# Optimization experiments

Hardware: AMD Instinct MI355X
Metric: run time of the kernel (lower is better)

## Reference

```python
import jax, jax.numpy as jnp
import numpy as np

EPS = 1e-8
BETA = 0.02          # bisector-band sharpness
ALPHA_UNION = 8.0    # exp-union strength
W_MIN, W_MAX = 0.005, 0.5
RAW_TEMP = 5.0       # width squash temperature
REL_TEMP = 0.05      # seed-relevance softmax temperature
A_MIN, A_MAX = 0.5, 2.0  # anisotropy eigenvalue range


def setup_inputs() -> dict:
    key = jax.random.key(0)
    k1, k2, k3, k4, k5 = jax.random.split(key, 5)
    N, S = 65536, 32
    return {
        "points_uv": jax.random.uniform(k1, (N, 2), dtype=jnp.float32),
        "seeds_raw": jax.random.uniform(k2, (S, 2), dtype=jnp.float32),
        "w_raw": jax.random.normal(k3, (1,), dtype=jnp.float32),
        "theta": jax.random.normal(k4, (S,), dtype=jnp.float32),
        "a_raw": jax.random.normal(k5, (S,), dtype=jnp.float32),
    }


def _metric_matrices(theta, a_raw):
    # anisotropic 2x2 SPD metrics M_s = R^T diag(a, 1/a) R
    t = jnp.tanh(a_raw)
    a = 0.5 * (A_MAX - A_MIN) * t + 0.5 * (A_MAX + A_MIN)  # (S,)
    c, s = jnp.cos(theta), jnp.sin(theta)
    R = jnp.stack([jnp.stack([c, -s], -1), jnp.stack([s, c], -1)], -2)  # (S,2,2)
    dvec = jnp.stack([a, 1.0 / (a + EPS)], -1)  # (S,2)
    return jnp.einsum("ska,sk,skb->sab", R, dvec, R)  # (S,2,2)


def reference(points_uv, seeds_raw, w_raw, theta, a_raw):
    S = seeds_raw.shape[0]
    # half-thickness around the Voronoi bisector
    w = W_MIN + (W_MAX - W_MIN) * jax.nn.sigmoid(w_raw[0] / RAW_TEMP)
    M = _metric_matrices(theta, a_raw)  # (S,2,2)

    # point-to-seed diffs with periodic wrapping on both u and v
    diff = points_uv[:, None, :] - seeds_raw[None, :, :]  # (N,S,2)
    diff = diff - jnp.round(diff)

    # anisotropic distances d_i(x) = sqrt(diff^T M_i diff)
    d = jnp.sqrt(jnp.einsum("nsa,sab,nsb->ns", diff, M, diff) + EPS)  # (N,S)

    # soft seed relevance -> soft pair weights P_ij (upper triangular, normalized)
    w_soft = jax.nn.softmax(-d / REL_TEMP, axis=1)  # (N,S)
    pair = w_soft[:, :, None] * w_soft[:, None, :]  # (N,S,S)
    mask = jnp.triu(jnp.ones((S, S), dtype=points_uv.dtype), k=1)
    pair = pair * mask
    P = pair / (pair.sum(axis=(1, 2), keepdims=True) + EPS)

    # bisector band: B_ij = sigmoid((w - |d_i - d_j|_smooth) / beta)
    Delta = d[:, :, None] - d[:, None, :]  # (N,S,S)
    abs_smooth = jnp.sqrt(Delta * Delta + EPS)
    B = jax.nn.sigmoid((w - abs_smooth) / BETA)

    # union over i<j pairs: rho = 1 - exp(-alpha * sum S_ij)
    S_sum = jnp.sum(P * B, axis=(1, 2))  # (N,)
    rho = 1.0 - jnp.exp(-ALPHA_UNION * S_sum)
    return rho
```

## Files before the change

kernel.cpp:

```cpp
#include <hip/hip_runtime.h>
#include <math.h>


#define LOG2E  1.4426950408889634f
#define EPSF   1e-8f
#define TSC    4096.0f
#define TAB_N  2816
#define HBAND  750
#define BLOCK  512
#define PPB    64
#define SSTR   40

__global__ __launch_bounds__(BLOCK, 8) void voronoi_v7(
    const float* __restrict__ points,
    const float* __restrict__ seeds,
    const float* __restrict__ w_raw,
    const float* __restrict__ theta,
    const float* __restrict__ a_raw,
    float* __restrict__ out,
    int N)
{
    __shared__ float    s_tab[TAB_N];
    __shared__ unsigned s_ii[PPB * SSTR];
    __shared__ float    s_ww[PPB * SSTR];
    __shared__ float    s_su[32], s_sv[32], s_m00[32], s_m01[32], s_m11[32];

    const int t = threadIdx.x;

    const float wr = w_raw[0];
    const float sg = __builtin_amdgcn_rcpf(1.0f + exp2f(wr * (-LOG2E / 5.0f)));
    const float w  = 0.005f + 0.495f * sg;

    const int icent = (int)(w * TSC + 0.5f);
    const int T1B   = (icent > HBAND ? icent - HBAND : 0) << 2;
    const int T2B   = (icent + HBAND) << 2;

    if (t < 32) {
        const float x  = a_raw[t];
        const float z  = exp2f(2.0f * LOG2E * x);
        const float th = (z - 1.0f) * __builtin_amdgcn_rcpf(z + 1.0f);
        const float a  = 0.75f * th + 1.25f;
        const float ia = __builtin_amdgcn_rcpf(a + EPSF);
        const float cs = __cosf(theta[t]);
        const float sn = __sinf(theta[t]);
        const float S2 = TSC * TSC;
        s_m00[t] = (a * cs * cs + ia * sn * sn) * S2;
        s_m01[t] = (2.0f * cs * sn * (ia - a)) * S2;
        s_m11[t] = (a * sn * sn + ia * cs * cs) * S2;
        s_su[t]  = seeds[2 * t];
        s_sv[t]  = seeds[2 * t + 1];
    }
    {
        const float kC = (50.0f * LOG2E) / TSC;
        const float kB = -w * (50.0f * LOG2E);
        #pragma unroll
        for (int k = t; k < TAB_N; k += BLOCK) {
            const float y = exp2f(fmaf((float)k, kC, kB));
            s_tab[k] = __builtin_amdgcn_rcpf(1.0f + y);
        }
    }
    __syncthreads();

    const int pb = t >> 3;
    const int g  = t & 7;
    const int s0 = g * 4;
    const int p  = blockIdx.x * PPB + pb;
    if (p >= N) return;

    const float4 su4  = *(const float4*)&s_su[s0];
    const float4 sv4  = *(const float4*)&s_sv[s0];
    const float4 m004 = *(const float4*)&s_m00[s0];
    const float4 m014 = *(const float4*)&s_m01[s0];
    const float4 m114 = *(const float4*)&s_m11[s0];

    const float2 uv = ((const float2*)points)[p];
    const float u = uv.x, v = uv.y;

    const float EPS_Q = 1e-8f * TSC * TSC;
    float4 d4;
#define DIST(SU, SV, M00, M01, M11, OUTD)                                  \
    {                                                                      \
        float du = u - (SU); du -= rintf(du);                              \
        float dv = v - (SV); dv -= rintf(dv);                              \
        float q = fmaf(du * du, (M00),                                     \
                  fmaf(du * dv, (M01),                                     \
                  fmaf(dv * dv, (M11), EPS_Q)));                           \
        (OUTD) = sqrtf(q);                                                 \
    }
    DIST(su4.x, sv4.x, m004.x, m014.x, m114.x, d4.x)
    DIST(su4.y, sv4.y, m004.y, m014.y, m114.y, d4.y)
    DIST(su4.z, sv4.z, m004.z, m014.z, m114.z, d4.z)
    DIST(su4.w, sv4.w, m004.w, m014.w, m114.w, d4.w)

    const float cE = -(20.0f * LOG2E) / TSC;
    float4 e4;
    e4.x = exp2f(d4.x * cE);
    e4.y = exp2f(d4.y * cE);
    e4.z = exp2f(d4.z * cE);
    e4.w = exp2f(d4.w * cE);
    float Z = (e4.x + e4.y) + (e4.z + e4.w);
    Z += __shfl_xor(Z, 1, 64);
    Z += __shfl_xor(Z, 2, 64);
    Z += __shfl_xor(Z, 4, 64);
    const float rcpZ = __builtin_amdgcn_rcpf(Z);
    float4 w4;
    w4.x = e4.x * rcpZ; w4.y = e4.y * rcpZ;
    w4.z = e4.z * rcpZ; w4.w = e4.w * rcpZ;
    float sumsq = w4.x * w4.x;
    sumsq = fmaf(w4.y, w4.y, sumsq);
    sumsq = fmaf(w4.z, w4.z, sumsq);
    sumsq = fmaf(w4.w, w4.w, sumsq);

    uint4 ii;
    ii.x = ((unsigned)(d4.x + 0.5f)) << 2;
    ii.y = ((unsigned)(d4.y + 0.5f)) << 2;
    ii.z = ((unsigned)(d4.z + 0.5f)) << 2;
    ii.w = ((unsigned)(d4.w + 0.5f)) << 2;

    unsigned* db = &s_ii[pb * SSTR];
    float*    wb = &s_ww[pb * SSTR];
    *(uint4*) (db + s0) = ii;
    *(float4*)(wb + s0) = w4;

    const char* tb = (const char*)s_tab;

#define TBODY(IA, IB, WJ, ACC)                                             \
    {                                                                      \
        const unsigned hi = (IA) > (IB) ? (IA) : (IB);                     \
        const unsigned lo = (IA) > (IB) ? (IB) : (IA);                     \
        int diff = (int)(hi - lo);                                         \
        diff = diff > T1B ? diff : T1B;                                    \
        diff = diff < T2B ? diff : T2B;                                    \
        const float B = *(const float*)(tb + diff);                        \
        (ACC) = fmaf((WJ), B, (ACC));                                      \
    }

    float b0, b1, b2, b3;
    b0 = 0.0f; b1 = 0.0f; b2 = 0.0f; b3 = 0.0f;
    TBODY(ii.x, ii.y, w4.y, b0)
    TBODY(ii.x, ii.z, w4.z, b0)
    TBODY(ii.x, ii.w, w4.w, b0)
    TBODY(ii.y, ii.z, w4.z, b1)
    TBODY(ii.y, ii.w, w4.w, b1)
    TBODY(ii.z, ii.w, w4.w, b2)

#define ROT(R)                                                             \
    {                                                                      \
        const int gj = ((g + (R)) & 7) * 4;                                \
        const uint4  ij = *(const uint4*) (db + gj);                       \
        const float4 wj = *(const float4*)(wb + gj);                       \
        TBODY(ii.x, ij.x, wj.x, b0)                                        \
        TBODY(ii.x, ij.y, wj.y, b0)                                        \
        TBODY(ii.x, ij.z, wj.z, b0)                                        \
        TBODY(ii.x, ij.w, wj.w, b0)                                        \
        TBODY(ii.y, ij.x, wj.x, b1)                                        \
        TBODY(ii.y, ij.y, wj.y, b1)                                        \
        TBODY(ii.y, ij.z, wj.z, b1)                                        \
        TBODY(ii.y, ij.w, wj.w, b1)                                        \
        TBODY(ii.z, ij.x, wj.x, b2)                                        \
        TBODY(ii.z, ij.y, wj.y, b2)                                        \
        TBODY(ii.z, ij.z, wj.z, b2)                                        \
        TBODY(ii.z, ij.w, wj.w, b2)                                        \
        TBODY(ii.w, ij.x, wj.x, b3)                                        \
        TBODY(ii.w, ij.y, wj.y, b3)                                        \
        TBODY(ii.w, ij.z, wj.z, b3)                                        \
        TBODY(ii.w, ij.w, wj.w, b3)                                        \
    }
    ROT(1)
    ROT(2)
    ROT(3)
    if (g < 4) {
        ROT(4)
    }

    float accb = w4.x * b0;
    accb = fmaf(w4.y, b1, accb);
    accb = fmaf(w4.z, b2, accb);
    accb = fmaf(w4.w, b3, accb);

    float nb = accb, sq = sumsq;
    nb += __shfl_xor(nb, 1, 64);  sq += __shfl_xor(sq, 1, 64);
    nb += __shfl_xor(nb, 2, 64);  sq += __shfl_xor(sq, 2, 64);
    nb += __shfl_xor(nb, 4, 64);  sq += __shfl_xor(sq, 4, 64);

    const float den   = fmaxf(0.5f * (1.0f - sq), 0.0f) + EPSF;
    const float ratio = nb * __builtin_amdgcn_rcpf(den);
    const float rho   = 1.0f - exp2f(ratio * (-8.0f * LOG2E));
    if (g == 0) out[p] = rho;
}

extern "C" void kernel_launch(void* const* d_in, const int* in_sizes, int n_in,
                              void* d_out, int out_size, void* d_ws, size_t ws_size,
                              hipStream_t stream) {
    const float* points = (const float*)d_in[0];
    const float* seeds  = (const float*)d_in[1];
    const float* w_raw  = (const float*)d_in[2];
    const float* theta  = (const float*)d_in[3];
    const float* a_raw  = (const float*)d_in[4];
    float* out = (float*)d_out;

    const int N = in_sizes[0] / 2;
    const int grid = (N + PPB - 1) / PPB;

    voronoi_v7<<<grid, BLOCK, 0, stream>>>(points, seeds, w_raw, theta, a_raw,
                                           out, N);
}
```

Before: 16.49 us.

## Replace dense sigmoid LDS table with lane-replicated bf16 piecewise-linear table

Swaps the fine-grained float sigmoid lookup table for a coarse 258-entry table. Each entry packs a bf16 base value and a bf16 slope and is stored 16 times, so each lane reads its own copy via t&15. Lookups then hit distinct LDS banks instead of gathering at random addresses and conflicting. In exchange, each pair does a few extra ALU ops to interpolate, precision drops to bf16 with linear interpolation, the explicit clamp band is gone, and the launch-bounds occupancy hint is removed.

```diff
diff --git a/kernel.cpp b/kernel.cpp
--- a/kernel.cpp
+++ b/kernel.cpp
@@ -5,13 +5,12 @@
 #define LOG2E  1.4426950408889634f
 #define EPSF   1e-8f
 #define TSC    4096.0f
-#define TAB_N  2816
-#define HBAND  750
+#define NTAB   258
 #define BLOCK  512
 #define PPB    64
 #define SSTR   40
 
-__global__ __launch_bounds__(BLOCK, 8) void voronoi_v7(
+__global__ __launch_bounds__(BLOCK) void voronoi_v9(
     const float* __restrict__ points,
     const float* __restrict__ seeds,
     const float* __restrict__ w_raw,
@@ -20,7 +19,7 @@
     float* __restrict__ out,
     int N)
 {
-    __shared__ float    s_tab[TAB_N];
+    __shared__ unsigned s_tab[NTAB * 16];
     __shared__ unsigned s_ii[PPB * SSTR];
     __shared__ float    s_ww[PPB * SSTR];
     __shared__ float    s_su[32], s_sv[32], s_m00[32], s_m01[32], s_m11[32];
@@ -30,10 +29,6 @@
     const float wr = w_raw[0];
     const float sg = __builtin_amdgcn_rcpf(1.0f + exp2f(wr * (-LOG2E / 5.0f)));
     const float w  = 0.005f + 0.495f * sg;
-
-    const int icent = (int)(w * TSC + 0.5f);
-    const int T1B   = (icent > HBAND ? icent - HBAND : 0) << 2;
-    const int T2B   = (icent + HBAND) << 2;
 
     if (t < 32) {
         const float x  = a_raw[t];
@@ -50,20 +45,29 @@
         s_su[t]  = seeds[2 * t];
         s_sv[t]  = seeds[2 * t + 1];
     }
-    {
-        const float kC = (50.0f * LOG2E) / TSC;
-        const float kB = -w * (50.0f * LOG2E);
+    if (t < NTAB) {
+        const float z0 = fmaf((float)t,       -50.0f / 256.0f, 50.0f * w);
+        const float z1 = fmaf((float)(t + 1), -50.0f / 256.0f, 50.0f * w);
+        const float y0 = exp2f(-z0 * LOG2E);
+        const float y1 = exp2f(-z1 * LOG2E);
+        const float sA = 1.0f / (1.0f + y0);
+        const float sB = 1.0f / (1.0f + y1);
+        const float sl = (sB - sA) * 0.0625f;
+        unsigned ua = __float_as_uint(sA);
+        ua = (ua + 0x7fffu + ((ua >> 16) & 1u)) >> 16;
+        unsigned ub = __float_as_uint(sl);
+        ub = (ub + 0x7fffu + ((ub >> 16) & 1u)) >> 16;
+        const unsigned pk = ua | (ub << 16);
+        const int base = t << 4;
         #pragma unroll
-        for (int k = t; k < TAB_N; k += BLOCK) {
-            const float y = exp2f(fmaf((float)k, kC, kB));
-            s_tab[k] = __builtin_amdgcn_rcpf(1.0f + y);
-        }
+        for (int c = 0; c < 16; ++c) s_tab[base + c] = pk;
     }
     __syncthreads();
 
     const int pb = t >> 3;
     const int g  = t & 7;
     const int s0 = g * 4;
+    const int cc = t & 15;
     const int p  = blockIdx.x * PPB + pb;
     if (p >= N) return;
 
@@ -112,26 +116,26 @@
     sumsq = fmaf(w4.w, w4.w, sumsq);
 
     uint4 ii;
-    ii.x = ((unsigned)(d4.x + 0.5f)) << 2;
-    ii.y = ((unsigned)(d4.y + 0.5f)) << 2;
-    ii.z = ((unsigned)(d4.z + 0.5f)) << 2;
-    ii.w = ((unsigned)(d4.w + 0.5f)) << 2;
+    ii.x = (unsigned)(d4.x + 0.5f);
+    ii.y = (unsigned)(d4.y + 0.5f);
+    ii.z = (unsigned)(d4.z + 0.5f);
+    ii.w = (unsigned)(d4.w + 0.5f);
 
     unsigned* db = &s_ii[pb * SSTR];
     float*    wb = &s_ww[pb * SSTR];
     *(uint4*) (db + s0) = ii;
     *(float4*)(wb + s0) = w4;
 
-    const char* tb = (const char*)s_tab;
-
 #define TBODY(IA, IB, WJ, ACC)                                             \
     {                                                                      \
         const unsigned hi = (IA) > (IB) ? (IA) : (IB);                     \
         const unsigned lo = (IA) > (IB) ? (IB) : (IA);                     \
-        int diff = (int)(hi - lo);                                         \
-        diff = diff > T1B ? diff : T1B;                                    \
-        diff = diff < T2B ? diff : T2B;                                    \
-        const float B = *(const float*)(tb + diff);                        \
+        const unsigned df = hi - lo;                                       \
+        const unsigned pk = s_tab[((df >> 4) << 4) + cc];                  \
+        const float fr    = (float)(df & 15u);                             \
+        const float base  = __uint_as_float(pk << 16);                     \
+        const float slope = __uint_as_float(pk & 0xffff0000u);             \
+        const float B     = fmaf(fr, slope, base);                         \
         (ACC) = fmaf((WJ), B, (ACC));                                      \
     }
 
@@ -202,6 +206,6 @@
     const int N = in_sizes[0] / 2;
     const int grid = (N + PPB - 1) / PPB;
 
-    voronoi_v7<<<grid, BLOCK, 0, stream>>>(points, seeds, w_raw, theta, a_raw,
+    voronoi_v9<<<grid, BLOCK, 0, stream>>>(points, seeds, w_raw, theta, a_raw,
                                            out, N);
 }
```

After: 19.26 us. 16.8% more time.
